# Kernel tuning notes

Measured on AMD Instinct MI355X. Metric: run time of the kernel, lower is better.

Reference implementation:

```python
import jax, jax.numpy as jnp
import numpy as np

N_HEAD = 16
N_KV_HEAD = 4
D_HEAD = 128
RMS_EPS = 1.1920929e-07  # torch default eps for fp32 rms_norm


def _rms_norm(x):
    return x * jax.lax.rsqrt(jnp.mean(x * x, axis=-1, keepdims=True) + RMS_EPS)


def _rotary_tables(n_pos, dim):
    # dim = d_head; freq table has dim//2 entries (half of them zero)
    angular_freq = (1.0 / 1024.0) ** jnp.linspace(0.0, 1.0, dim // 4, dtype=jnp.float32)
    angular_freq = jnp.concatenate([angular_freq, jnp.zeros(dim // 4, jnp.float32)])
    theta = jnp.arange(n_pos, dtype=jnp.float32)[:, None] * angular_freq[None, :]
    return jnp.cos(theta), jnp.sin(theta)


def _apply_rotary(x):
    # x: (B, H, T, D). Faithful to source: cos/sin indexed by x.shape[-3] (= H),
    # broadcast over the time axis.
    n = x.shape[-3]
    cos, sin = _rotary_tables(n, x.shape[-1])
    cos = cos[None, :, None, :]
    sin = sin[None, :, None, :]
    xf = x.astype(jnp.float32)
    x1, x2 = jnp.split(xf, 2, axis=-1)
    y1 = x1 * cos + x2 * sin
    y2 = -x1 * sin + x2 * cos
    return jnp.concatenate([y1, y2], axis=-1).astype(x.dtype)


def setup_inputs() -> dict:
    key = jax.random.key(0)
    k1, k2, k3, k4 = jax.random.split(key, 4)
    B, T, C = 2, 2048, 2048
    return {
        "x": jax.random.normal(k1, (B, T, C), jnp.float32),
        "Wq": jax.random.normal(k2, (C, C), jnp.float32) * 0.02,
        "Wkv": jax.random.normal(k3, (2 * N_KV_HEAD * D_HEAD, C), jnp.float32) * 0.02,
        "Wproj": jax.random.normal(k4, (C, C), jnp.float32) * 0.02,
        "tok_masks": jnp.ones((B, T), jnp.int32),
    }


def reference(x, Wq, Wkv, Wproj, tok_masks):
    B, T, C = x.shape
    nh, nkv, dh = N_HEAD, N_KV_HEAD, D_HEAD

    q = (x @ Wq.T).reshape(B, T, nh, dh).transpose(0, 2, 1, 3)          # (B,nh,T,dh)
    kv = x @ Wkv.T                                                       # (B,T,2*nkv*dh)
    k, v = jnp.split(kv, 2, axis=2)
    k = k.reshape(B, T, nkv, dh).transpose(0, 2, 1, 3)                   # (B,nkv,T,dh)
    v = v.reshape(B, T, nkv, dh).transpose(0, 2, 1, 3)

    q, k = _rms_norm(q), _rms_norm(k)
    q, k = _apply_rotary(q), _apply_rotary(k)

    # GQA: repeat kv heads to match query heads
    rep = nh // nkv
    k = jnp.repeat(k, rep, axis=1)
    v = jnp.repeat(v, rep, axis=1)

    scale = 1.0 / jnp.sqrt(jnp.float32(dh))
    scores = jnp.einsum("bhqd,bhkd->bhqk", q, k) * scale                 # (B,nh,T,T)
    causal = jnp.tril(jnp.ones((T, T), bool))
    scores = jnp.where(causal[None, None], scores, -jnp.inf)
    attn = jax.nn.softmax(scores, axis=-1)
    y = jnp.einsum("bhqk,bhkd->bhqd", attn, v)                           # (B,nh,T,dh)
    y = y.transpose(0, 2, 1, 3).reshape(B, T, C)
    y = y @ Wproj.T
    return (y, jnp.float32(0.0))
```

## Files before the change

kernel.cpp:

```cpp
#include <hip/hip_runtime.h>
#include <hip/hip_bf16.h>

#define T_SEQ 2048
#define BATCH 2
#define CDIM  2048
#define NH    16
#define NKV   4
#define DH    128

typedef __attribute__((ext_vector_type(8))) short bfrag;
typedef __attribute__((ext_vector_type(4))) float ffrag;
typedef __hip_bfloat16 bf16;

#if defined(__has_builtin)
#if __has_builtin(__builtin_amdgcn_global_load_lds)
#define USE_GLL 1
#endif
#endif
#ifndef USE_GLL
#define USE_GLL 0
#endif

__device__ __forceinline__ void stage16(const bf16* __restrict__ g, bf16* lds_base, int lane) {
#if USE_GLL
    __builtin_amdgcn_global_load_lds((const __attribute__((address_space(1))) void*)g,
                                     (__attribute__((address_space(3))) void*)lds_base, 16, 0, 0);
#else
    *(bfrag*)(lds_base + lane * 8) = *(const bfrag*)g;
#endif
}

struct bf16x4 { bf16 a, b, c, d; };
__global__ void cast_f2b(const float* __restrict__ src, bf16* __restrict__ dst, int n4) {
    int i = blockIdx.x * blockDim.x + threadIdx.x;
    if (i < n4) {
        float4 f = ((const float4*)src)[i];
        bf16x4 o{__float2bfloat16(f.x), __float2bfloat16(f.y),
                 __float2bfloat16(f.z), __float2bfloat16(f.w)};
        ((bf16x4*)dst)[i] = o;
    }
}

template<int MODE>
__global__ __launch_bounds__(256) void gemm_k(
    const bf16* __restrict__ A, const bf16* __restrict__ W,
    bf16* __restrict__ out0, bf16* __restrict__ out1, float* __restrict__ outf)
{
    __shared__ __align__(16) bf16 sA[128 * 32];
    __shared__ __align__(16) bf16 sB[128 * 32];
    const int lane = threadIdx.x & 63;
    const int w = threadIdx.x >> 6;
    const int m0 = blockIdx.x * 128, n0 = blockIdx.y * 128;
    const int lr = lane & 15, quad = lane >> 4, lk = quad * 8;
    const int m_off = (w & 1) * 64, n_off = (w >> 1) * 64;

    const bf16* ap = A + (size_t)(m0 + w * 32 + (lane >> 2)) * CDIM + (lane & 3) * 8;
    const bf16* bp = W + (size_t)(n0 + w * 32 + (lane >> 2)) * CDIM + (lane & 3) * 8;
    bf16* sA0 = &sA[(w * 32) * 32];
    bf16* sA1 = &sA[(w * 32 + 16) * 32];
    bf16* sB0 = &sB[(w * 32) * 32];
    bf16* sB1 = &sB[(w * 32 + 16) * 32];

    ffrag acc[4][4] = {};
    for (int kk = 0; kk < CDIM; kk += 32) {
        __syncthreads();
        stage16(ap, sA0, lane);
        stage16(ap + (size_t)16 * CDIM, sA1, lane);
        stage16(bp, sB0, lane);
        stage16(bp + (size_t)16 * CDIM, sB1, lane);
        ap += 32; bp += 32;
        __syncthreads();

        bfrag af[4], bg[4];
        #pragma unroll
        for (int s = 0; s < 4; ++s) af[s] = *(const bfrag*)&sA[(m_off + s * 16 + lr) * 32 + lk];
        #pragma unroll
        for (int s = 0; s < 4; ++s) bg[s] = *(const bfrag*)&sB[(n_off + s * 16 + lr) * 32 + lk];
        #pragma unroll
        for (int i = 0; i < 4; ++i)
            #pragma unroll
            for (int j = 0; j < 4; ++j)
                acc[i][j] = __builtin_amdgcn_mfma_f32_16x16x32_bf16(af[i], bg[j], acc[i][j], 0, 0, 0);
    }

    #pragma unroll
    for (int si = 0; si < 4; ++si) {
        #pragma unroll
        for (int sj = 0; sj < 4; ++sj) {
            #pragma unroll
            for (int i = 0; i < 4; ++i) {
                int m = m0 + m_off + si * 16 + quad * 4 + i;
                int n = n0 + n_off + sj * 16 + lr;
                float v = acc[si][sj][i];
                if (MODE == 0) {
                    int b = m >> 11, t = m & (T_SEQ - 1);
                    int h = n >> 7, d = n & (DH - 1);
                    out0[(((size_t)(b * NH + h) * T_SEQ + t) << 7) + d] = __float2bfloat16(v);
                } else if (MODE == 1) {
                    int b = m >> 11, t = m & (T_SEQ - 1);
                    if (n < NKV * DH) {
                        int h = n >> 7, d = n & (DH - 1);
                        out0[(((size_t)(b * NKV + h) * T_SEQ + t) << 7) + d] = __float2bfloat16(v);
                    } else {
                        int n2 = n - NKV * DH;
                        int h = n2 >> 7, d = n2 & (DH - 1);
                        out1[(((size_t)(b * NKV + h) * DH + d) << 11) + t] = __float2bfloat16(v);
                    }
                } else {
                    outf[(size_t)m * CDIM + n] = v;
                }
            }
        }
    }
    if (MODE == 2 && blockIdx.x == 0 && blockIdx.y == 0 && threadIdx.x == 0) {
        outf[(size_t)BATCH * T_SEQ * CDIM] = 0.0f;
    }
}

__global__ __launch_bounds__(256) void normrope_k(bf16* __restrict__ buf, int nheads) {
    const int row = blockIdx.x * 4 + (threadIdx.x >> 6);
    const int h = (row >> 11) % nheads;
    bf16* p = buf + (size_t)row * DH;
    const int d = threadIdx.x & 63;
    float x1 = __bfloat162float(p[d]);
    float x2 = __bfloat162float(p[d + 64]);
    float ss = x1 * x1 + x2 * x2;
    #pragma unroll
    for (int off = 32; off; off >>= 1) ss += __shfl_xor(ss, off);
    float r = rsqrtf(ss * (1.0f / 128.0f) + 1.1920929e-07f);
    x1 *= r; x2 *= r;
    float freq = (d < 32) ? exp2f(-10.0f * (float)d * (1.0f / 31.0f)) : 0.0f;
    float th = (float)h * freq;
    float c, s;
    __sincosf(th, &s, &c);
    p[d]      = __float2bfloat16(x1 * c + x2 * s);
    p[d + 64] = __float2bfloat16(-x1 * s + x2 * c);
}

#define PSTR 72
#define KSTR 136
#define VSTR 72
__global__ __launch_bounds__(256) void attn_k(const bf16* __restrict__ Q, const bf16* __restrict__ K,
                                              const bf16* __restrict__ VT, bf16* __restrict__ Y)
{
    const int lane = threadIdx.x & 63;
    const int w = threadIdx.x >> 6;
    const int p = blockIdx.x, h = blockIdx.y, b = blockIdx.z;
    const int lr = lane & 15, quad = lane >> 4, lk = quad * 8;
    const bf16* Qb = Q  + (size_t)(b * NH  + h)        * T_SEQ * DH;
    const bf16* Kb = K  + (size_t)(b * NKV + (h >> 2)) * T_SEQ * DH;
    const bf16* Vb = VT + (size_t)(b * NKV + (h >> 2)) * DH * T_SEQ;

    __shared__ __align__(16) bf16 SK[64 * KSTR];
    __shared__ __align__(16) bf16 SV[128 * VSTR];
    __shared__ __align__(16) bf16 SP[4][16 * PSTR];
    bf16* Pl = SP[w];

    const int krow = w * 16 + (lane >> 4);
    const int kcol = (lane & 15) * 8;
    const int vrow = w * 32 + (lane >> 3);
    const int vcol = (lane & 7) * 8;
    const float scale = 0.08838834764831845f;

    for (int pass = 0; pass < 2; ++pass) {
        const int qblk = pass ? (31 - p) : p;
        const int nc = qblk + 1;
        const int q0 = qblk * 64 + w * 16;

        bfrag qf[4];
        #pragma unroll
        for (int dc = 0; dc < 4; ++dc)
            qf[dc] = *(const bfrag*)(Qb + (size_t)(q0 + lr) * DH + dc * 32 + lk);

        float lp[4] = {0.f, 0.f, 0.f, 0.f};
        ffrag o[8] = {};

        bfrag kr[4], vr[4];
        #pragma unroll
        for (int j = 0; j < 4; ++j) {
            kr[j] = *(const bfrag*)(Kb + (size_t)(krow + j * 4) * DH + kcol);
            vr[j] = *(const bfrag*)(Vb + (size_t)(vrow + j * 8) * T_SEQ + vcol);
        }

        for (int c = 0; c < nc; ++c) {
            const int base = c * 64;
            __syncthreads();
            #pragma unroll
            for (int j = 0; j < 4; ++j) {
                *(bfrag*)&SK[(size_t)(w * 16 + j * 4 + (lane >> 4)) * KSTR + kcol] = kr[j];
                *(bfrag*)&SV[(size_t)(w * 32 + j * 8 + (lane >> 3)) * VSTR + vcol] = vr[j];
            }
            if (c + 1 < nc) {
                const int nb = base + 64;
                #pragma unroll
                for (int j = 0; j < 4; ++j) {
                    kr[j] = *(const bfrag*)(Kb + (size_t)(nb + krow + j * 4) * DH + kcol);
                    vr[j] = *(const bfrag*)(Vb + (size_t)(vrow + j * 8) * T_SEQ + nb + vcol);
                }
            }
            __syncthreads();

            ffrag s[4] = {};
            #pragma unroll
            for (int kt = 0; kt < 4; ++kt) {
                const bf16* kp = &SK[(kt * 16 + lr) * KSTR + lk];
                #pragma unroll
                for (int dc = 0; dc < 4; ++dc)
                    s[kt] = __builtin_amdgcn_mfma_f32_16x16x32_bf16(qf[dc], *(const bfrag*)(kp + dc * 32), s[kt], 0, 0, 0);
            }

            if (c == qblk) {
                #pragma unroll
                for (int kt = 0; kt < 4; ++kt) {
                    const int col = base + kt * 16 + lr;
                    #pragma unroll
                    for (int i = 0; i < 4; ++i) {
                        const int row = q0 + quad * 4 + i;
                        float e = (col <= row) ? __expf(fmaf(s[kt][i], scale, -16.0f)) : 0.0f;
                        lp[i] += e;
                        Pl[(quad * 4 + i) * PSTR + kt * 16 + lr] = __float2bfloat16(e);
                    }
                }
            } else {
                #pragma unroll
                for (int kt = 0; kt < 4; ++kt) {
                    #pragma unroll
                    for (int i = 0; i < 4; ++i) {
                        float e = __expf(fmaf(s[kt][i], scale, -16.0f));
                        lp[i] += e;
                        Pl[(quad * 4 + i) * PSTR + kt * 16 + lr] = __float2bfloat16(e);
                    }
                }
            }

            const bfrag pf0 = *(const bfrag*)&Pl[lr * PSTR + lk];
            const bfrag pf1 = *(const bfrag*)&Pl[lr * PSTR + 32 + lk];
            #pragma unroll
            for (int dt = 0; dt < 8; ++dt) {
                const bf16* vp = &SV[(dt * 16 + lr) * VSTR + lk];
                o[dt] = __builtin_amdgcn_mfma_f32_16x16x32_bf16(pf0, *(const bfrag*)vp, o[dt], 0, 0, 0);
                o[dt] = __builtin_amdgcn_mfma_f32_16x16x32_bf16(pf1, *(const bfrag*)(vp + 32), o[dt], 0, 0, 0);
            }
        }

        float inv[4];
        #pragma unroll
        for (int i = 0; i < 4; ++i) {
            float l = lp[i];
            #pragma unroll
            for (int off = 1; off < 16; off <<= 1) l += __shfl_xor(l, off);
            inv[i] = 1.0f / l;
        }
        #pragma unroll
        for (int dt = 0; dt < 8; ++dt)
            #pragma unroll
            for (int i = 0; i < 4; ++i) {
                int row = q0 + quad * 4 + i;
                Y[((size_t)(b * T_SEQ) + row) * CDIM + h * DH + dt * 16 + lr] = __float2bfloat16(o[dt][i] * inv[i]);
            }
    }
}

extern "C" void kernel_launch(void* const* d_in, const int* in_sizes, int n_in,
                              void* d_out, int out_size, void* d_ws, size_t ws_size,
                              hipStream_t stream) {
    const float* x     = (const float*)d_in[0];
    const float* Wq    = (const float*)d_in[1];
    const float* Wkv   = (const float*)d_in[2];
    const float* Wproj = (const float*)d_in[3];
    float* out = (float*)d_out;

    char* ws = (char*)d_ws;
    size_t off = 0;
    auto alloc = [&](size_t bytes) { void* p = ws + off; off += (bytes + 255) & ~255ULL; return p; };
    bf16* xb   = (bf16*)alloc((size_t)BATCH * T_SEQ * CDIM * 2);
    bf16* wqb  = (bf16*)alloc((size_t)CDIM * CDIM * 2);
    bf16* wkvb = (bf16*)alloc((size_t)2 * NKV * DH * CDIM * 2);
    bf16* wpb  = (bf16*)alloc((size_t)CDIM * CDIM * 2);
    bf16* qb   = (bf16*)alloc((size_t)BATCH * NH * T_SEQ * DH * 2);
    bf16* kb   = (bf16*)alloc((size_t)BATCH * NKV * T_SEQ * DH * 2);
    bf16* vtb  = (bf16*)alloc((size_t)BATCH * NKV * DH * T_SEQ * 2);
    bf16* y1   = (bf16*)alloc((size_t)BATCH * T_SEQ * CDIM * 2);

    int n;
    n = BATCH * T_SEQ * CDIM / 4; cast_f2b<<<(n + 255) / 256, 256, 0, stream>>>(x, xb, n);
    n = CDIM * CDIM / 4;          cast_f2b<<<(n + 255) / 256, 256, 0, stream>>>(Wq, wqb, n);
    n = 2 * NKV * DH * CDIM / 4;  cast_f2b<<<(n + 255) / 256, 256, 0, stream>>>(Wkv, wkvb, n);
    n = CDIM * CDIM / 4;          cast_f2b<<<(n + 255) / 256, 256, 0, stream>>>(Wproj, wpb, n);

    gemm_k<0><<<dim3(32, 16), 256, 0, stream>>>(xb, wqb, qb, nullptr, nullptr);
    gemm_k<1><<<dim3(32, 8),  256, 0, stream>>>(xb, wkvb, kb, vtb, nullptr);
    normrope_k<<<BATCH * NH * T_SEQ / 4,  256, 0, stream>>>(qb, NH);
    normrope_k<<<BATCH * NKV * T_SEQ / 4, 256, 0, stream>>>(kb, NKV);
    attn_k<<<dim3(16, NH, BATCH), 256, 0, stream>>>(qb, kb, vtb, y1);
    gemm_k<2><<<dim3(32, 16), 256, 0, stream>>>(y1, wpb, nullptr, nullptr, out);
}
```

Baseline: 347.9 us.

## Merge cast and QKV launches, double query rows per attention wave

The four fp32-to-bf16 cast launches become one kernel, and the Q and KV projection GEMMs become one launch with a 32x24 grid. The attention kernel now has each wave own 32 query rows (two 16-row tiles), so the block covers 128 queries. Each K/V fragment read from LDS feeds twice as many MFMAs, and the P tile uses a permuted row layout. This halves the attention grid (256 blocks) and raises register pressure, which may cut occupancy and hurt latency hiding.

```diff
diff --git a/kernel.cpp b/kernel.cpp
--- a/kernel.cpp
+++ b/kernel.cpp
@@ -31,26 +31,42 @@
 }
 
 struct bf16x4 { bf16 a, b, c, d; };
-__global__ void cast_f2b(const float* __restrict__ src, bf16* __restrict__ dst, int n4) {
-    int i = blockIdx.x * blockDim.x + threadIdx.x;
-    if (i < n4) {
-        float4 f = ((const float4*)src)[i];
-        bf16x4 o{__float2bfloat16(f.x), __float2bfloat16(f.y),
-                 __float2bfloat16(f.z), __float2bfloat16(f.w)};
-        ((bf16x4*)dst)[i] = o;
+#define N4_X   (BATCH * T_SEQ * CDIM / 4)
+#define N4_WQ  (CDIM * CDIM / 4)
+#define N4_WKV (2 * NKV * DH * CDIM / 4)
+#define N4_WP  (CDIM * CDIM / 4)
+__global__ __launch_bounds__(256) void cast_all(
+    const float* __restrict__ x, const float* __restrict__ wq,
+    const float* __restrict__ wkv, const float* __restrict__ wp,
+    bf16* __restrict__ xb, bf16* __restrict__ wqb, bf16* __restrict__ wkvb, bf16* __restrict__ wpb)
+{
+    int j = blockIdx.x * 256 + threadIdx.x;
+    const float* s; bf16* d;
+    if (j < N4_X) { s = x; d = xb; }
+    else {
+        j -= N4_X;
+        if (j < N4_WQ) { s = wq; d = wqb; }
+        else {
+            j -= N4_WQ;
+            if (j < N4_WKV) { s = wkv; d = wkvb; }
+            else { j -= N4_WKV; if (j >= N4_WP) return; s = wp; d = wpb; }
+        }
     }
+    float4 f = ((const float4*)s)[j];
+    bf16x4 o{__float2bfloat16(f.x), __float2bfloat16(f.y),
+             __float2bfloat16(f.z), __float2bfloat16(f.w)};
+    ((bf16x4*)d)[j] = o;
 }
 
 template<int MODE>
-__global__ __launch_bounds__(256) void gemm_k(
-    const bf16* __restrict__ A, const bf16* __restrict__ W,
+__device__ __forceinline__ void gemm_body(
+    const bf16* __restrict__ A, const bf16* __restrict__ W, int m0, int n0,
     bf16* __restrict__ out0, bf16* __restrict__ out1, float* __restrict__ outf)
 {
     __shared__ __align__(16) bf16 sA[128 * 32];
     __shared__ __align__(16) bf16 sB[128 * 32];
     const int lane = threadIdx.x & 63;
     const int w = threadIdx.x >> 6;
-    const int m0 = blockIdx.x * 128, n0 = blockIdx.y * 128;
     const int lr = lane & 15, quad = lane >> 4, lk = quad * 8;
     const int m_off = (w & 1) * 64, n_off = (w >> 1) * 64;
 
@@ -112,9 +128,24 @@
             }
         }
     }
-    if (MODE == 2 && blockIdx.x == 0 && blockIdx.y == 0 && threadIdx.x == 0) {
+}
+
+__global__ __launch_bounds__(256) void gemm_qkv(
+    const bf16* __restrict__ A, const bf16* __restrict__ Wq, const bf16* __restrict__ Wkv,
+    bf16* __restrict__ q, bf16* __restrict__ k, bf16* __restrict__ vt)
+{
+    if (blockIdx.y < 16)
+        gemm_body<0>(A, Wq, blockIdx.x * 128, blockIdx.y * 128, q, nullptr, nullptr);
+    else
+        gemm_body<1>(A, Wkv, blockIdx.x * 128, (blockIdx.y - 16) * 128, k, vt, nullptr);
+}
+
+__global__ __launch_bounds__(256) void gemm_proj(
+    const bf16* __restrict__ A, const bf16* __restrict__ W, float* __restrict__ outf)
+{
+    gemm_body<2>(A, W, blockIdx.x * 128, blockIdx.y * 128, nullptr, nullptr, outf);
+    if (blockIdx.x == 0 && blockIdx.y == 0 && threadIdx.x == 0)
         outf[(size_t)BATCH * T_SEQ * CDIM] = 0.0f;
-    }
 }
 
 __global__ __launch_bounds__(256) void normrope_k(bf16* __restrict__ buf, int nheads) {
@@ -153,27 +184,29 @@
 
     __shared__ __align__(16) bf16 SK[64 * KSTR];
     __shared__ __align__(16) bf16 SV[128 * VSTR];
-    __shared__ __align__(16) bf16 SP[4][16 * PSTR];
-    bf16* Pl = SP[w];
+    __shared__ __align__(16) bf16 SP[4][2][16 * PSTR];
 
     const int krow = w * 16 + (lane >> 4);
     const int kcol = (lane & 15) * 8;
     const int vrow = w * 32 + (lane >> 3);
     const int vcol = (lane & 7) * 8;
+    const int prow = ((lr & 3) << 2) | (lr >> 2);
     const float scale = 0.08838834764831845f;
 
     for (int pass = 0; pass < 2; ++pass) {
-        const int qblk = pass ? (31 - p) : p;
-        const int nc = qblk + 1;
-        const int q0 = qblk * 64 + w * 16;
-
-        bfrag qf[4];
-        #pragma unroll
-        for (int dc = 0; dc < 4; ++dc)
-            qf[dc] = *(const bfrag*)(Qb + (size_t)(q0 + lr) * DH + dc * 32 + lk);
-
-        float lp[4] = {0.f, 0.f, 0.f, 0.f};
-        ffrag o[8] = {};
+        const int qb = pass ? (15 - p) : p;
+        const int nc = 2 * (qb + 1);
+        const int q0 = qb * 128 + w * 32;
+
+        bfrag qf[2][4];
+        #pragma unroll
+        for (int t = 0; t < 2; ++t)
+            #pragma unroll
+            for (int dc = 0; dc < 4; ++dc)
+                qf[t][dc] = *(const bfrag*)(Qb + (size_t)(q0 + t * 16 + lr) * DH + dc * 32 + lk);
+
+        float lp[2][4] = {};
+        ffrag o[2][8] = {};
 
         bfrag kr[4], vr[4];
         #pragma unroll
@@ -187,8 +220,8 @@
             __syncthreads();
             #pragma unroll
             for (int j = 0; j < 4; ++j) {
-                *(bfrag*)&SK[(size_t)(w * 16 + j * 4 + (lane >> 4)) * KSTR + kcol] = kr[j];
-                *(bfrag*)&SV[(size_t)(w * 32 + j * 8 + (lane >> 3)) * VSTR + vcol] = vr[j];
+                *(bfrag*)&SK[(size_t)(krow + j * 4) * KSTR + kcol] = kr[j];
+                *(bfrag*)&SV[(size_t)(vrow + j * 8) * VSTR + vcol] = vr[j];
             }
             if (c + 1 < nc) {
                 const int nb = base + 64;
@@ -200,64 +233,73 @@
             }
             __syncthreads();
 
-            ffrag s[4] = {};
+            ffrag s[2][4] = {};
             #pragma unroll
             for (int kt = 0; kt < 4; ++kt) {
                 const bf16* kp = &SK[(kt * 16 + lr) * KSTR + lk];
                 #pragma unroll
-                for (int dc = 0; dc < 4; ++dc)
-                    s[kt] = __builtin_amdgcn_mfma_f32_16x16x32_bf16(qf[dc], *(const bfrag*)(kp + dc * 32), s[kt], 0, 0, 0);
-            }
-
-            if (c == qblk) {
+                for (int dc = 0; dc < 4; ++dc) {
+                    bfrag kf = *(const bfrag*)(kp + dc * 32);
+                    s[0][kt] = __builtin_amdgcn_mfma_f32_16x16x32_bf16(qf[0][dc], kf, s[0][kt], 0, 0, 0);
+                    s[1][kt] = __builtin_amdgcn_mfma_f32_16x16x32_bf16(qf[1][dc], kf, s[1][kt], 0, 0, 0);
+                }
+            }
+
+            const bool maskc = (c >= 2 * qb);
+            #pragma unroll
+            for (int t = 0; t < 2; ++t) {
+                bf16* Pl = SP[w][t];
                 #pragma unroll
                 for (int kt = 0; kt < 4; ++kt) {
                     const int col = base + kt * 16 + lr;
                     #pragma unroll
                     for (int i = 0; i < 4; ++i) {
-                        const int row = q0 + quad * 4 + i;
-                        float e = (col <= row) ? __expf(fmaf(s[kt][i], scale, -16.0f)) : 0.0f;
-                        lp[i] += e;
-                        Pl[(quad * 4 + i) * PSTR + kt * 16 + lr] = __float2bfloat16(e);
+                        const int row = q0 + t * 16 + quad * 4 + i;
+                        float e = (!maskc || col <= row) ? __expf(fmaf(s[t][kt][i], scale, -16.0f)) : 0.0f;
+                        lp[t][i] += e;
+                        Pl[(i * 4 + quad) * PSTR + kt * 16 + lr] = __float2bfloat16(e);
                     }
                 }
-            } else {
-                #pragma unroll
-                for (int kt = 0; kt < 4; ++kt) {
-                    #pragma unroll
-                    for (int i = 0; i < 4; ++i) {
-                        float e = __expf(fmaf(s[kt][i], scale, -16.0f));
-                        lp[i] += e;
-                        Pl[(quad * 4 + i) * PSTR + kt * 16 + lr] = __float2bfloat16(e);
-                    }
-                }
-            }
-
-            const bfrag pf0 = *(const bfrag*)&Pl[lr * PSTR + lk];
-            const bfrag pf1 = *(const bfrag*)&Pl[lr * PSTR + 32 + lk];
+            }
+
+            bfrag pf[2][2];
+            #pragma unroll
+            for (int t = 0; t < 2; ++t) {
+                pf[t][0] = *(const bfrag*)&SP[w][t][prow * PSTR + lk];
+                pf[t][1] = *(const bfrag*)&SP[w][t][prow * PSTR + 32 + lk];
+            }
             #pragma unroll
             for (int dt = 0; dt < 8; ++dt) {
                 const bf16* vp = &SV[(dt * 16 + lr) * VSTR + lk];
-                o[dt] = __builtin_amdgcn_mfma_f32_16x16x32_bf16(pf0, *(const bfrag*)vp, o[dt], 0, 0, 0);
-                o[dt] = __builtin_amdgcn_mfma_f32_16x16x32_bf16(pf1, *(const bfrag*)(vp + 32), o[dt], 0, 0, 0);
-            }
-        }
-
-        float inv[4];
-        #pragma unroll
-        for (int i = 0; i < 4; ++i) {
-            float l = lp[i];
-            #pragma unroll
-            for (int off = 1; off < 16; off <<= 1) l += __shfl_xor(l, off);
-            inv[i] = 1.0f / l;
-        }
-        #pragma unroll
-        for (int dt = 0; dt < 8; ++dt)
+                bfrag vf0 = *(const bfrag*)vp;
+                bfrag vf1 = *(const bfrag*)(vp + 32);
+                #pragma unroll
+                for (int t = 0; t < 2; ++t) {
+                    o[t][dt] = __builtin_amdgcn_mfma_f32_16x16x32_bf16(pf[t][0], vf0, o[t][dt], 0, 0, 0);
+                    o[t][dt] = __builtin_amdgcn_mfma_f32_16x16x32_bf16(pf[t][1], vf1, o[t][dt], 0, 0, 0);
+                }
+            }
+        }
+
+        #pragma unroll
+        for (int t = 0; t < 2; ++t) {
+            float inv[4];
             #pragma unroll
             for (int i = 0; i < 4; ++i) {
-                int row = q0 + quad * 4 + i;
-                Y[((size_t)(b * T_SEQ) + row) * CDIM + h * DH + dt * 16 + lr] = __float2bfloat16(o[dt][i] * inv[i]);
-            }
+                float l = lp[t][i];
+                #pragma unroll
+                for (int off = 1; off < 16; off <<= 1) l += __shfl_xor(l, off);
+                inv[i] = 1.0f / l;
+            }
+            #pragma unroll
+            for (int dt = 0; dt < 8; ++dt)
+                #pragma unroll
+                for (int i = 0; i < 4; ++i) {
+                    int row = q0 + t * 16 + quad * 4 + i;
+                    Y[((size_t)(b * T_SEQ) + row) * CDIM + h * DH + dt * 16 + lr] =
+                        __float2bfloat16(o[t][dt][i] * inv[i]);
+                }
+        }
     }
 }
 
@@ -282,16 +324,12 @@
     bf16* vtb  = (bf16*)alloc((size_t)BATCH * NKV * DH * T_SEQ * 2);
     bf16* y1   = (bf16*)alloc((size_t)BATCH * T_SEQ * CDIM * 2);
 
-    int n;
-    n = BATCH * T_SEQ * CDIM / 4; cast_f2b<<<(n + 255) / 256, 256, 0, stream>>>(x, xb, n);
-    n = CDIM * CDIM / 4;          cast_f2b<<<(n + 255) / 256, 256, 0, stream>>>(Wq, wqb, n);
-    n = 2 * NKV * DH * CDIM / 4;  cast_f2b<<<(n + 255) / 256, 256, 0, stream>>>(Wkv, wkvb, n);
-    n = CDIM * CDIM / 4;          cast_f2b<<<(n + 255) / 256, 256, 0, stream>>>(Wproj, wpb, n);
-
-    gemm_k<0><<<dim3(32, 16), 256, 0, stream>>>(xb, wqb, qb, nullptr, nullptr);
-    gemm_k<1><<<dim3(32, 8),  256, 0, stream>>>(xb, wkvb, kb, vtb, nullptr);
+    const int total4 = N4_X + N4_WQ + N4_WKV + N4_WP;
+    cast_all<<<(total4 + 255) / 256, 256, 0, stream>>>(x, Wq, Wkv, Wproj, xb, wqb, wkvb, wpb);
+
+    gemm_qkv<<<dim3(32, 24), 256, 0, stream>>>(xb, wqb, wkvb, qb, kb, vtb);
     normrope_k<<<BATCH * NH * T_SEQ / 4,  256, 0, stream>>>(qb, NH);
     normrope_k<<<BATCH * NKV * T_SEQ / 4, 256, 0, stream>>>(kb, NKV);
-    attn_k<<<dim3(16, NH, BATCH), 256, 0, stream>>>(qb, kb, vtb, y1);
-    gemm_k<2><<<dim3(32, 16), 256, 0, stream>>>(y1, wpb, nullptr, nullptr, out);
-}
+    attn_k<<<dim3(8, NH, BATCH), 256, 0, stream>>>(qb, kb, vtb, y1);
+    gemm_proj<<<dim3(32, 16), 256, 0, stream>>>(y1, wpb, out);
+}
```

Result: faster. 314.3 us (-9.7%).
